# Kernel optimization log

Hardware: AMD Instinct MI355X
Metric: run time of the kernel (lower is better)

The kernel has to match this reference:

```python
import jax, jax.numpy as jnp
import numpy as np
import math

EMBED_DIM = 1024
NUM_HEADS = 16
HEAD_DIM = EMBED_DIM // NUM_HEADS
BLOCK_SIZE = 64
N_GLOBAL = 8


def _sparse_mask(seq_len: int) -> jnp.ndarray:
    """Block-diagonal local mask + 8 global tokens (rows and cols), bool [S, S]."""
    idx = jnp.arange(seq_len)
    block_id = idx // BLOCK_SIZE
    local = block_id[:, None] == block_id[None, :]
    # torch.linspace(0, S-1, min(8, S)).long() -> truncated evenly spaced positions
    gp = np.linspace(0, seq_len - 1, min(N_GLOBAL, seq_len)).astype(np.int64)
    is_global = jnp.zeros((seq_len,), dtype=bool).at[jnp.asarray(gp)].set(True)
    return local | is_global[:, None] | is_global[None, :]


def setup_inputs() -> dict:
    key = jax.random.key(0)
    ks = jax.random.split(key, 9)
    E = EMBED_DIM
    s = 0.02
    return {
        "x": jax.random.normal(ks[0], (1, 4096, E), dtype=jnp.float32),
        "Wq": jax.random.normal(ks[1], (E, E), dtype=jnp.float32) * s,
        "bq": jnp.zeros((E,), dtype=jnp.float32),
        "Wk": jax.random.normal(ks[2], (E, E), dtype=jnp.float32) * s,
        "bk": jnp.zeros((E,), dtype=jnp.float32),
        "Wv": jax.random.normal(ks[3], (E, E), dtype=jnp.float32) * s,
        "bv": jnp.zeros((E,), dtype=jnp.float32),
        "Wo": jax.random.normal(ks[4], (E, E), dtype=jnp.float32) * s,
        "bo": jnp.zeros((E,), dtype=jnp.float32),
    }


def reference(x, Wq, bq, Wk, bk, Wv, bv, Wo, bo):
    B, S, E = x.shape
    H, D = NUM_HEADS, HEAD_DIM
    mask = _sparse_mask(S)  # [S, S] bool

    def split_heads(y):
        return y.reshape(B, S, H, D).transpose(0, 2, 1, 3)  # [B,H,S,D]

    q = split_heads(x @ Wq + bq)
    k = split_heads(x @ Wk + bk)
    v = split_heads(x @ Wv + bv)

    scale = math.sqrt(D)
    scores = jnp.einsum("bhqd,bhkd->bhqk", q, k) / scale  # [B,H,S,S]
    scores = jnp.where(mask[None, None], scores, -jnp.inf)
    attn = jax.nn.softmax(scores, axis=-1)  # every row has its diagonal block -> no NaN
    out = jnp.einsum("bhqk,bhkd->bhqd", attn, v)
    out = out.transpose(0, 2, 1, 3).reshape(B, S, E)
    return out @ Wo + bo
```

## Files before the change

### kernel.cpp

```cpp
#include <hip/hip_runtime.h>

typedef __attribute__((ext_vector_type(8))) short short8;
typedef __attribute__((ext_vector_type(8))) __bf16 bf16x8;
typedef __attribute__((ext_vector_type(4))) float f32x4;

#define S_LEN 4096
#define EMB   1024
#define NHEAD 16
#define HDIM  64
#define GCHUNK 256
#define NCHUNK (S_LEN / GCHUNK)

__constant__ int GPOS[8] = {0, 585, 1170, 1755, 2340, 2925, 3510, 4095};

__device__ __forceinline__ unsigned short f2bf(float f) {
    unsigned int u = __float_as_uint(f);
    u += 0x7fffu + ((u >> 16) & 1u);
    return (unsigned short)(u >> 16);
}
__device__ __forceinline__ float bf2f(unsigned short s) {
    return __uint_as_float(((unsigned int)s) << 16);
}
#define GLOAD16(src, dst) __builtin_amdgcn_global_load_lds( \
    (const __attribute__((address_space(1))) void*)(src),    \
    (__attribute__((address_space(3))) void*)(dst), 16, 0, 0)

__global__ __launch_bounds__(256) void convert_x_kernel(const float4* __restrict__ in,
                                                        ushort4* __restrict__ out, int n4) {
    for (int i = blockIdx.x * blockDim.x + threadIdx.x; i < n4; i += gridDim.x * blockDim.x) {
        float4 v = in[i];
        ushort4 o;
        o.x = f2bf(v.x); o.y = f2bf(v.y); o.z = f2bf(v.z); o.w = f2bf(v.w);
        out[i] = o;
    }
}

__global__ __launch_bounds__(256) void convert_w_kernel(const float* __restrict__ W0,
                                                        const float* __restrict__ W1,
                                                        const float* __restrict__ W2,
                                                        const float* __restrict__ W3,
                                                        unsigned short* __restrict__ wt) {
    __shared__ float tile[64][65];
    const int bx = blockIdx.x;
    const int w = bx >> 8, rem = bx & 255;
    const int k0 = (rem >> 4) * 64, n0 = (rem & 15) * 64;
    const float* W = (w == 0) ? W0 : (w == 1) ? W1 : (w == 2) ? W2 : W3;
    unsigned short* dst = wt + (size_t)w * (1u << 20);
    const int t = threadIdx.x;
    for (int i = t; i < 4096; i += 256) {
        int r = i >> 6, c = i & 63;
        tile[r][c] = W[(size_t)(k0 + r) * EMB + n0 + c];
    }
    __syncthreads();
    for (int i = t; i < 4096; i += 256) {
        int r = i >> 6, c = i & 63;
        dst[(size_t)(n0 + r) * EMB + k0 + c] = f2bf(tile[c][r]);
    }
}

__global__ __launch_bounds__(256) void vtrans(const unsigned short* __restrict__ vb,
                                              unsigned short* __restrict__ vtg) {
    __shared__ unsigned short tile[64][72];
    const int t = threadIdx.x;
    const int h = blockIdx.x >> 6;
    const int s0 = (blockIdx.x & 63) * 64;
    for (int i = t; i < 512; i += 256) {
        int r = i >> 3, c = i & 7;
        *(short8*)&tile[r][c * 8] = *(const short8*)(vb + (size_t)(s0 + r) * EMB + h * 64 + c * 8);
    }
    __syncthreads();
    for (int i = t; i < 512; i += 256) {
        int d = i >> 3, c = i & 7;
        short8 v;
#pragma unroll
        for (int j = 0; j < 8; ++j) v[j] = (short)tile[c * 8 + j][d];
        *(short8*)(vtg + (size_t)(h * 64 + d) * S_LEN + s0 + c * 8) = v;
    }
}

__global__ __launch_bounds__(256) void gemm_qkv(const unsigned short* __restrict__ A,
                                                const unsigned short* __restrict__ Bt,
                                                const float* __restrict__ bq,
                                                const float* __restrict__ bk,
                                                const float* __restrict__ bv,
                                                unsigned short* __restrict__ qb,
                                                unsigned short* __restrict__ kb,
                                                unsigned short* __restrict__ vb) {
    __shared__ unsigned short As[2][128 * 64];
    __shared__ unsigned short Bs[2][128 * 64];
    const int t = threadIdx.x;
    const int lane = t & 63;
    const int wave = t >> 6;
    const int wm = wave >> 1, wn = wave & 1;
    const int col16 = lane & 15, grp = lane >> 4;
    const int bm = blockIdx.x / 24;
    const int bn = blockIdx.x % 24;
    const int sel = bn >> 3, bn_l = bn & 7;
    const float* bias = (sel == 0) ? bq : (sel == 1) ? bk : bv;
    unsigned short* out = (sel == 0) ? qb : (sel == 1) ? kb : vb;

    f32x4 acc[4][4] = {};

    auto stage = [&](int buf, int tstep) {
        const int k0 = tstep * 64;
#pragma unroll
        for (int c = 0; c < 4; ++c) {
            int p = t + 256 * c;
            int row = p >> 3, s = p & 7, kc = s ^ (row & 7);
            GLOAD16(A + (size_t)(bm * 128 + row) * EMB + k0 + kc * 8, &As[buf][p * 8]);
        }
#pragma unroll
        for (int c = 0; c < 4; ++c) {
            int p = t + 256 * c;
            int row = p >> 3, s = p & 7, kc = s ^ (row & 7);
            GLOAD16(Bt + (size_t)(bn * 128 + row) * EMB + k0 + kc * 8, &Bs[buf][p * 8]);
        }
    };

    auto compute = [&](int cur) {
        const unsigned short* Ab = As[cur];
        const unsigned short* Bb = Bs[cur];
#pragma unroll
        for (int kk = 0; kk < 2; ++kk) {
            const int kc = kk * 4 + grp;
            bf16x8 af[4], bfr[4];
#pragma unroll
            for (int f = 0; f < 4; ++f) {
                int mrow = wm * 64 + f * 16 + col16;
                short8 ra = *(const short8*)(Ab + (mrow * 8 + (kc ^ (mrow & 7))) * 8);
                af[f] = __builtin_bit_cast(bf16x8, ra);
                int nrow = wn * 64 + f * 16 + col16;
                short8 rb = *(const short8*)(Bb + (nrow * 8 + (kc ^ (nrow & 7))) * 8);
                bfr[f] = __builtin_bit_cast(bf16x8, rb);
            }
#pragma unroll
            for (int fi = 0; fi < 4; ++fi)
#pragma unroll
                for (int fj = 0; fj < 4; ++fj)
                    acc[fi][fj] = __builtin_amdgcn_mfma_f32_16x16x32_bf16(af[fi], bfr[fj], acc[fi][fj], 0, 0, 0);
        }
    };

    stage(0, 0);
    stage(1, 1);

#pragma unroll 2
    for (int tstep = 0; tstep < 14; ++tstep) {
        const int cur = tstep & 1;
        asm volatile("s_waitcnt vmcnt(8)" ::: "memory");
        __builtin_amdgcn_s_barrier();
        compute(cur);
        __builtin_amdgcn_s_barrier();
        stage(cur, tstep + 2);
    }
    asm volatile("s_waitcnt vmcnt(8)" ::: "memory");
    __builtin_amdgcn_s_barrier();
    compute(0);
    asm volatile("s_waitcnt vmcnt(0)" ::: "memory");
    __builtin_amdgcn_s_barrier();
    compute(1);

#pragma unroll
    for (int fi = 0; fi < 4; ++fi) {
        const int row0 = bm * 128 + wm * 64 + fi * 16 + grp * 4;
#pragma unroll
        for (int fj = 0; fj < 4; ++fj) {
            const int col = bn_l * 128 + wn * 64 + fj * 16 + col16;
            const float bvv = bias[col];
#pragma unroll
            for (int r = 0; r < 4; ++r)
                out[(size_t)(row0 + r) * EMB + col] = f2bf(acc[fi][fj][r] + bvv);
        }
    }
}

__global__ __launch_bounds__(256) void gemm_out(const unsigned short* __restrict__ A,
                                                const unsigned short* __restrict__ Bt,
                                                const float* __restrict__ bias,
                                                float* __restrict__ Cout) {
    __shared__ unsigned short As[2][128 * 64];
    __shared__ unsigned short Bs[2][128 * 64];
    const int t = threadIdx.x;
    const int lane = t & 63;
    const int wave = t >> 6;
    const int wm = wave >> 1, wn = wave & 1;
    const int col16 = lane & 15, grp = lane >> 4;
    const int bm = blockIdx.x >> 3;
    const int bn = blockIdx.x & 7;

    f32x4 acc[4][4] = {};

    auto stage = [&](int buf, int tstep) {
        const int k0 = tstep * 64;
#pragma unroll
        for (int c = 0; c < 4; ++c) {
            int p = t + 256 * c;
            int row = p >> 3, s = p & 7, kc = s ^ (row & 7);
            GLOAD16(A + (size_t)(bm * 128 + row) * EMB + k0 + kc * 8, &As[buf][p * 8]);
        }
#pragma unroll
        for (int c = 0; c < 4; ++c) {
            int p = t + 256 * c;
            int row = p >> 3, s = p & 7, kc = s ^ (row & 7);
            GLOAD16(Bt + (size_t)(bn * 128 + row) * EMB + k0 + kc * 8, &Bs[buf][p * 8]);
        }
    };

    auto compute = [&](int cur) {
        const unsigned short* Ab = As[cur];
        const unsigned short* Bb = Bs[cur];
#pragma unroll
        for (int kk = 0; kk < 2; ++kk) {
            const int kc = kk * 4 + grp;
            bf16x8 af[4], bfr[4];
#pragma unroll
            for (int f = 0; f < 4; ++f) {
                int mrow = wm * 64 + f * 16 + col16;
                short8 ra = *(const short8*)(Ab + (mrow * 8 + (kc ^ (mrow & 7))) * 8);
                af[f] = __builtin_bit_cast(bf16x8, ra);
                int nrow = wn * 64 + f * 16 + col16;
                short8 rb = *(const short8*)(Bb + (nrow * 8 + (kc ^ (nrow & 7))) * 8);
                bfr[f] = __builtin_bit_cast(bf16x8, rb);
            }
#pragma unroll
            for (int fi = 0; fi < 4; ++fi)
#pragma unroll
                for (int fj = 0; fj < 4; ++fj)
                    acc[fi][fj] = __builtin_amdgcn_mfma_f32_16x16x32_bf16(af[fi], bfr[fj], acc[fi][fj], 0, 0, 0);
        }
    };

    stage(0, 0);
    stage(1, 1);

#pragma unroll 2
    for (int tstep = 0; tstep < 14; ++tstep) {
        const int cur = tstep & 1;
        asm volatile("s_waitcnt vmcnt(8)" ::: "memory");
        __builtin_amdgcn_s_barrier();
        compute(cur);
        __builtin_amdgcn_s_barrier();
        stage(cur, tstep + 2);
    }
    asm volatile("s_waitcnt vmcnt(8)" ::: "memory");
    __builtin_amdgcn_s_barrier();
    compute(0);
    asm volatile("s_waitcnt vmcnt(0)" ::: "memory");
    __builtin_amdgcn_s_barrier();
    compute(1);

#pragma unroll
    for (int fi = 0; fi < 4; ++fi) {
        const int row0 = bm * 128 + wm * 64 + fi * 16 + grp * 4;
#pragma unroll
        for (int fj = 0; fj < 4; ++fj) {
            const int col = bn * 128 + wn * 64 + fj * 16 + col16;
            const float bvv = bias[col];
#pragma unroll
            for (int r = 0; r < 4; ++r)
                Cout[(size_t)(row0 + r) * EMB + col] = acc[fi][fj][r] + bvv;
        }
    }
}

__global__ __launch_bounds__(256) void attn_local(const unsigned short* __restrict__ qb,
                                                  const unsigned short* __restrict__ kb,
                                                  const unsigned short* __restrict__ vb,
                                                  const unsigned short* __restrict__ vtg,
                                                  unsigned short* __restrict__ ab) {
    __shared__ unsigned short Qs[64 * 64];
    __shared__ unsigned short Ks[80 * 64];
    __shared__ unsigned short Vts[64 * 64];
    __shared__ unsigned short Ps[64 * 64];
    __shared__ float Pg[64][9];
    __shared__ float Vg[8][64];

    const int t = threadIdx.x;
    const int lane = t & 63, wave = t >> 6;
    const int col16 = lane & 15, grp = lane >> 4;
    const int h = blockIdx.x >> 6, b = blockIdx.x & 63;
    const int bc = h * 64;

#pragma unroll
    for (int c = 0; c < 2; ++c) {
        int p = t + 256 * c, row = p >> 3, s = p & 7, kc = s ^ (row & 7);
        GLOAD16(qb + (size_t)(b * 64 + row) * EMB + bc + kc * 8, Qs + p * 8);
    }
#pragma unroll
    for (int c = 0; c < 3; ++c) {
        int p = t + 256 * c;
        if (p < 576) {
            int row = p >> 3, s = p & 7, kc = s ^ (row & 7);
            int srow = (row < 64) ? (b * 64 + row) : GPOS[row - 64];
            GLOAD16(kb + (size_t)srow * EMB + bc + kc * 8, Ks + p * 8);
        }
    }
    if (t < 64) {
        short8 z = {};
        *(short8*)(Ks + (576 + t) * 8) = z;
    }
#pragma unroll
    for (int c = 0; c < 2; ++c) {
        int p = t + 256 * c, row = p >> 3, s = p & 7, kc = s ^ (row & 7);
        GLOAD16(vtg + (size_t)(bc + row) * S_LEN + b * 64 + kc * 8, Vts + p * 8);
    }
    for (int i = t; i < 512; i += 256) {
        int g = i >> 6, d = i & 63;
        Vg[g][d] = bf2f(vb[(size_t)GPOS[g] * EMB + bc + d]);
    }
    asm volatile("s_waitcnt vmcnt(0)" ::: "memory");
    __syncthreads();

    f32x4 sc[5] = {};
    const int arow = wave * 16 + col16;
#pragma unroll
    for (int kk = 0; kk < 2; ++kk) {
        const int kc = kk * 4 + (lane >> 4);
        short8 ra = *(const short8*)(Qs + (arow * 8 + (kc ^ (arow & 7))) * 8);
        bf16x8 af = __builtin_bit_cast(bf16x8, ra);
#pragma unroll
        for (int n = 0; n < 5; ++n) {
            const int brow = n * 16 + col16;
            short8 rb = *(const short8*)(Ks + (brow * 8 + (kc ^ (brow & 7))) * 8);
            sc[n] = __builtin_amdgcn_mfma_f32_16x16x32_bf16(af, __builtin_bit_cast(bf16x8, rb), sc[n], 0, 0, 0);
        }
    }

    const bool valid4 = (col16 < 8) && ((GPOS[col16] >> 6) != b);
#pragma unroll
    for (int r = 0; r < 4; ++r) {
        const int row = wave * 16 + grp * 4 + r;
        float s[5];
#pragma unroll
        for (int n = 0; n < 4; ++n) s[n] = sc[n][r] * 0.125f;
        s[4] = valid4 ? sc[4][r] * 0.125f : -1e30f;
        float m = fmaxf(fmaxf(fmaxf(s[0], s[1]), fmaxf(s[2], s[3])), s[4]);
#pragma unroll
        for (int off = 1; off < 16; off <<= 1) m = fmaxf(m, __shfl_xor(m, off));
        float e[5], l = 0.f;
#pragma unroll
        for (int n = 0; n < 5; ++n) { e[n] = __expf(s[n] - m); l += e[n]; }
#pragma unroll
        for (int off = 1; off < 16; off <<= 1) l += __shfl_xor(l, off);
        const float inv = 1.f / l;
#pragma unroll
        for (int n = 0; n < 4; ++n) {
            const int col = n * 16 + col16;
            const int kc = col >> 3;
            Ps[(row * 8 + (kc ^ (row & 7))) * 8 + (col & 7)] = f2bf(e[n] * inv);
        }
        if (col16 < 8) Pg[row][col16] = e[4] * inv;
    }
    __syncthreads();

    f32x4 oa[4] = {};
#pragma unroll
    for (int kk = 0; kk < 2; ++kk) {
        const int kc = kk * 4 + (lane >> 4);
        short8 ra = *(const short8*)(Ps + (arow * 8 + (kc ^ (arow & 7))) * 8);
        bf16x8 af = __builtin_bit_cast(bf16x8, ra);
#pragma unroll
        for (int n = 0; n < 4; ++n) {
            const int drow = n * 16 + col16;
            short8 rb = *(const short8*)(Vts + (drow * 8 + (kc ^ (drow & 7))) * 8);
            oa[n] = __builtin_amdgcn_mfma_f32_16x16x32_bf16(af, __builtin_bit_cast(bf16x8, rb), oa[n], 0, 0, 0);
        }
    }

    float pgr[4][8];
#pragma unroll
    for (int r = 0; r < 4; ++r) {
        const int row = wave * 16 + grp * 4 + r;
#pragma unroll
        for (int g = 0; g < 8; ++g) pgr[r][g] = Pg[row][g];
    }
#pragma unroll
    for (int n = 0; n < 4; ++n) {
        const int d = n * 16 + col16;
#pragma unroll
        for (int g = 0; g < 8; ++g) {
            const float vg = Vg[g][d];
#pragma unroll
            for (int r = 0; r < 4; ++r) oa[n][r] += pgr[r][g] * vg;
        }
    }

#pragma unroll
    for (int n = 0; n < 4; ++n) {
        const int d = n * 16 + col16;
#pragma unroll
        for (int r = 0; r < 4; ++r) {
            const int row = wave * 16 + grp * 4 + r;
            ab[(size_t)(b * 64 + row) * EMB + bc + d] = f2bf(oa[n][r]);
        }
    }
}

__global__ __launch_bounds__(256) void attn_gpart(const unsigned short* __restrict__ qb,
                                                  const unsigned short* __restrict__ kb,
                                                  const unsigned short* __restrict__ vb,
                                                  float* __restrict__ o_part,
                                                  float* __restrict__ m_l) {
    __shared__ float Qs[8][64];
    __shared__ unsigned short Vs[GCHUNK][64];
    __shared__ float Ps[8][GCHUNK];
    __shared__ float mfin[8], lfin[8];
    const int t = threadIdx.x;
    const int lane = t & 63;
    const int wave = t >> 6;
    const int h = blockIdx.x >> 4;
    const int ch = blockIdx.x & (NCHUNK - 1);
    const int bc = h * 64;
    const int k0 = ch * GCHUNK;

    for (int i = t; i < 512; i += 256) {
        int r = i >> 6, d = i & 63;
        Qs[r][d] = bf2f(qb[(size_t)GPOS[r] * EMB + bc + d]);
    }
    {
        const unsigned short* vrow = vb + (size_t)(k0 + t) * EMB + bc;
#pragma unroll
        for (int c = 0; c < 8; ++c) {
            short8 vv = *(const short8*)(vrow + c * 8);
            *(short8*)(&Vs[t][(c ^ (t & 7)) * 8]) = vv;
        }
    }
    float kf[64];
    {
        const unsigned short* krow = kb + (size_t)(k0 + t) * EMB + bc;
#pragma unroll
        for (int c = 0; c < 8; ++c) {
            short8 kv = *(const short8*)(krow + c * 8);
#pragma unroll
            for (int j = 0; j < 8; ++j) kf[c * 8 + j] = bf2f((unsigned short)kv[j]);
        }
    }
    __syncthreads();

#pragma unroll
    for (int r = 0; r < 8; ++r) {
        float a0 = 0.f, a1 = 0.f, a2 = 0.f, a3 = 0.f;
#pragma unroll
        for (int c4 = 0; c4 < 16; ++c4) {
            f32x4 q = *(const f32x4*)&Qs[r][c4 * 4];
            a0 += q.x * kf[c4 * 4 + 0];
            a1 += q.y * kf[c4 * 4 + 1];
            a2 += q.z * kf[c4 * 4 + 2];
            a3 += q.w * kf[c4 * 4 + 3];
        }
        Ps[r][t] = (a0 + a1 + a2 + a3) * 0.125f;
    }
    __syncthreads();

#pragma unroll
    for (int rr = 0; rr < 2; ++rr) {
        const int r = wave * 2 + rr;
        float v0 = Ps[r][lane], v1 = Ps[r][lane + 64], v2 = Ps[r][lane + 128], v3 = Ps[r][lane + 192];
        float m = fmaxf(fmaxf(v0, v1), fmaxf(v2, v3));
#pragma unroll
        for (int off = 1; off < 64; off <<= 1) m = fmaxf(m, __shfl_xor(m, off));
        float e0 = __expf(v0 - m), e1 = __expf(v1 - m), e2 = __expf(v2 - m), e3 = __expf(v3 - m);
        float l = e0 + e1 + e2 + e3;
#pragma unroll
        for (int off = 1; off < 64; off <<= 1) l += __shfl_xor(l, off);
        Ps[r][lane] = e0; Ps[r][lane + 64] = e1; Ps[r][lane + 128] = e2; Ps[r][lane + 192] = e3;
        if (lane == 0) { mfin[r] = m; lfin[r] = l; }
    }
    __syncthreads();

    const int r = t >> 5;
    const int d0 = (t & 31) * 2;
    const int cc = d0 >> 3, ee = d0 & 7;
    float acc0 = 0.f, acc1 = 0.f;
    for (int k = 0; k < GCHUNK; k += 4) {
        f32x4 p = *(const f32x4*)&Ps[r][k];
#pragma unroll
        for (int j = 0; j < 4; ++j) {
            unsigned int vv = *(const unsigned int*)&Vs[k + j][((cc ^ ((k + j) & 7)) << 3) + ee];
            acc0 += p[j] * bf2f((unsigned short)(vv & 0xffff));
            acc1 += p[j] * bf2f((unsigned short)(vv >> 16));
        }
    }
    const int rowg = h * 8 + r;
    float* od = o_part + ((size_t)rowg * NCHUNK + ch) * 64 + d0;
    od[0] = acc0; od[1] = acc1;
    if ((t & 31) == 0) {
        m_l[((size_t)rowg * NCHUNK + ch) * 2 + 0] = mfin[r];
        m_l[((size_t)rowg * NCHUNK + ch) * 2 + 1] = lfin[r];
    }
}

__global__ __launch_bounds__(256) void attn_gcomb(const float* __restrict__ o_part,
                                                  const float* __restrict__ m_l,
                                                  unsigned short* __restrict__ ab) {
    const int gid = blockIdx.x * 256 + threadIdx.x;
    const int row = gid >> 6, d = gid & 63;
    float M = -1e30f;
#pragma unroll
    for (int c = 0; c < NCHUNK; ++c) M = fmaxf(M, m_l[((size_t)row * NCHUNK + c) * 2]);
    float L = 0.f, o = 0.f;
#pragma unroll
    for (int c = 0; c < NCHUNK; ++c) {
        float w = __expf(m_l[((size_t)row * NCHUNK + c) * 2] - M);
        L += m_l[((size_t)row * NCHUNK + c) * 2 + 1] * w;
        o += o_part[((size_t)row * NCHUNK + c) * 64 + d] * w;
    }
    const int h = row >> 3, gi = row & 7;
    ab[(size_t)GPOS[gi] * EMB + h * 64 + d] = f2bf(o / L);
}

extern "C" void kernel_launch(void* const* d_in, const int* in_sizes, int n_in,
                              void* d_out, int out_size, void* d_ws, size_t ws_size,
                              hipStream_t stream) {
    const float* x  = (const float*)d_in[0];
    const float* Wq = (const float*)d_in[1];
    const float* bq = (const float*)d_in[2];
    const float* Wk = (const float*)d_in[3];
    const float* bk = (const float*)d_in[4];
    const float* Wv = (const float*)d_in[5];
    const float* bv = (const float*)d_in[6];
    const float* Wo = (const float*)d_in[7];
    const float* bo = (const float*)d_in[8];

    char* ws = (char*)d_ws;
    unsigned short* xb = (unsigned short*)ws;
    unsigned short* wt = (unsigned short*)(ws + (8u << 20));
    unsigned short* qb = (unsigned short*)(ws + (16u << 20));
    unsigned short* kb = (unsigned short*)(ws + (24u << 20));
    unsigned short* vb = (unsigned short*)(ws + (32u << 20));
    unsigned short* ab = xb;

    float* o_part = (float*)d_out;
    float* m_l    = (float*)d_out + 128 * NCHUNK * 64;
    unsigned short* vtg = (unsigned short*)((char*)d_out + (4u << 20));

    const int n4 = S_LEN * EMB / 4;
    convert_x_kernel<<<2048, 256, 0, stream>>>((const float4*)x, (ushort4*)xb, n4);
    convert_w_kernel<<<1024, 256, 0, stream>>>(Wq, Wk, Wv, Wo, wt);

    gemm_qkv<<<(S_LEN / 128) * 24, 256, 0, stream>>>(xb, wt, bq, bk, bv, qb, kb, vb);

    vtrans<<<1024, 256, 0, stream>>>(vb, vtg);
    attn_local<<<NHEAD * 64, 256, 0, stream>>>(qb, kb, vb, vtg, ab);
    attn_gpart<<<NHEAD * NCHUNK, 256, 0, stream>>>(qb, kb, vb, o_part, m_l);
    attn_gcomb<<<(128 * 64) / 256, 256, 0, stream>>>(o_part, m_l, ab);

    gemm_out<<<(S_LEN / 128) * 8, 256, 0, stream>>>(ab, wt + (3u << 20), bo, (float*)d_out);
}
```

Measured before the change: 101.2 us.

## Fuse conversions, V transpose into QKV epilogue, and attention kernels

Merges the x and weight conversion kernels into one launch, folds the V transpose into the QKV GEMM epilogue via a swizzled LDS tile, and merges local and global-row attention kernels into one grid branching on block index. This removes three kernel launches, the separate vtrans pass over V, and lets the small global-attention work overlap with local attention. The fused attention kernel uses a shared LDS buffer sized for the larger path, which may affect occupancy, and V blocks of the GEMM do extra LDS work and stores.

```diff
diff --git a/kernel.cpp b/kernel.cpp
--- a/kernel.cpp
+++ b/kernel.cpp
@@ -25,56 +25,39 @@
     (const __attribute__((address_space(1))) void*)(src),    \
     (__attribute__((address_space(3))) void*)(dst), 16, 0, 0)
 
-__global__ __launch_bounds__(256) void convert_x_kernel(const float4* __restrict__ in,
-                                                        ushort4* __restrict__ out, int n4) {
-    for (int i = blockIdx.x * blockDim.x + threadIdx.x; i < n4; i += gridDim.x * blockDim.x) {
-        float4 v = in[i];
-        ushort4 o;
-        o.x = f2bf(v.x); o.y = f2bf(v.y); o.z = f2bf(v.z); o.w = f2bf(v.w);
-        out[i] = o;
-    }
-}
-
-__global__ __launch_bounds__(256) void convert_w_kernel(const float* __restrict__ W0,
-                                                        const float* __restrict__ W1,
-                                                        const float* __restrict__ W2,
-                                                        const float* __restrict__ W3,
-                                                        unsigned short* __restrict__ wt) {
+__global__ __launch_bounds__(256) void convert_all(const float* __restrict__ x,
+                                                   const float* __restrict__ W0,
+                                                   const float* __restrict__ W1,
+                                                   const float* __restrict__ W2,
+                                                   const float* __restrict__ W3,
+                                                   ushort4* __restrict__ xb,
+                                                   unsigned short* __restrict__ wt) {
     __shared__ float tile[64][65];
-    const int bx = blockIdx.x;
-    const int w = bx >> 8, rem = bx & 255;
-    const int k0 = (rem >> 4) * 64, n0 = (rem & 15) * 64;
-    const float* W = (w == 0) ? W0 : (w == 1) ? W1 : (w == 2) ? W2 : W3;
-    unsigned short* dst = wt + (size_t)w * (1u << 20);
     const int t = threadIdx.x;
-    for (int i = t; i < 4096; i += 256) {
-        int r = i >> 6, c = i & 63;
-        tile[r][c] = W[(size_t)(k0 + r) * EMB + n0 + c];
-    }
-    __syncthreads();
-    for (int i = t; i < 4096; i += 256) {
-        int r = i >> 6, c = i & 63;
-        dst[(size_t)(n0 + r) * EMB + k0 + c] = f2bf(tile[c][r]);
-    }
-}
-
-__global__ __launch_bounds__(256) void vtrans(const unsigned short* __restrict__ vb,
-                                              unsigned short* __restrict__ vtg) {
-    __shared__ unsigned short tile[64][72];
-    const int t = threadIdx.x;
-    const int h = blockIdx.x >> 6;
-    const int s0 = (blockIdx.x & 63) * 64;
-    for (int i = t; i < 512; i += 256) {
-        int r = i >> 3, c = i & 7;
-        *(short8*)&tile[r][c * 8] = *(const short8*)(vb + (size_t)(s0 + r) * EMB + h * 64 + c * 8);
-    }
-    __syncthreads();
-    for (int i = t; i < 512; i += 256) {
-        int d = i >> 3, c = i & 7;
-        short8 v;
-#pragma unroll
-        for (int j = 0; j < 8; ++j) v[j] = (short)tile[c * 8 + j][d];
-        *(short8*)(vtg + (size_t)(h * 64 + d) * S_LEN + s0 + c * 8) = v;
+    if (blockIdx.x < 1024) {
+        const int bx = blockIdx.x;
+        const int w = bx >> 8, rem = bx & 255;
+        const int k0 = (rem >> 4) * 64, n0 = (rem & 15) * 64;
+        const float* W = (w == 0) ? W0 : (w == 1) ? W1 : (w == 2) ? W2 : W3;
+        unsigned short* dst = wt + (size_t)w * (1u << 20);
+        for (int i = t; i < 4096; i += 256) {
+            int r = i >> 6, c = i & 63;
+            tile[r][c] = W[(size_t)(k0 + r) * EMB + n0 + c];
+        }
+        __syncthreads();
+        for (int i = t; i < 4096; i += 256) {
+            int r = i >> 6, c = i & 63;
+            dst[(size_t)(n0 + r) * EMB + k0 + c] = f2bf(tile[c][r]);
+        }
+    } else {
+        const int n4 = S_LEN * EMB / 4;
+        const float4* in = (const float4*)x;
+        for (int i = (blockIdx.x - 1024) * 256 + t; i < n4; i += 2048 * 256) {
+            float4 v = in[i];
+            ushort4 o;
+            o.x = f2bf(v.x); o.y = f2bf(v.y); o.z = f2bf(v.z); o.w = f2bf(v.w);
+            xb[i] = o;
+        }
     }
 }
 
@@ -85,7 +68,8 @@
                                                 const float* __restrict__ bv,
                                                 unsigned short* __restrict__ qb,
                                                 unsigned short* __restrict__ kb,
-                                                unsigned short* __restrict__ vb) {
+                                                unsigned short* __restrict__ vb,
+                                                unsigned short* __restrict__ vtg) {
     __shared__ unsigned short As[2][128 * 64];
     __shared__ unsigned short Bs[2][128 * 64];
     const int t = threadIdx.x;
@@ -170,6 +154,31 @@
 #pragma unroll
             for (int r = 0; r < 4; ++r)
                 out[(size_t)(row0 + r) * EMB + col] = f2bf(acc[fi][fj][r] + bvv);
+        }
+    }
+
+    if (sel == 2) {
+        __syncthreads();
+        unsigned short* T = &As[0][0];
+#pragma unroll
+        for (int fi = 0; fi < 4; ++fi) {
+            const int row_l = wm * 64 + fi * 16 + grp * 4;
+#pragma unroll
+            for (int fj = 0; fj < 4; ++fj) {
+                const int col_l = wn * 64 + fj * 16 + col16;
+                const float bvv = bias[bn_l * 128 + col_l];
+#pragma unroll
+                for (int r = 0; r < 4; ++r)
+                    T[col_l * 128 + ((row_l + r) ^ ((col_l & 15) << 3))] = f2bf(acc[fi][fj][r] + bvv);
+            }
+        }
+        __syncthreads();
+#pragma unroll
+        for (int c = 0; c < 8; ++c) {
+            int q = t + 256 * c;
+            int col = q >> 4, sc = q & 15, s0 = sc * 8;
+            short8 v = *(const short8*)(T + col * 128 + (s0 ^ ((col & 15) << 3)));
+            *(short8*)(vtg + (size_t)(bn_l * 128 + col) * S_LEN + bm * 128 + s0) = v;
         }
     }
 }
@@ -263,230 +272,232 @@
     }
 }
 
-__global__ __launch_bounds__(256) void attn_local(const unsigned short* __restrict__ qb,
+__global__ __launch_bounds__(256) void attn_fused(const unsigned short* __restrict__ qb,
                                                   const unsigned short* __restrict__ kb,
                                                   const unsigned short* __restrict__ vb,
                                                   const unsigned short* __restrict__ vtg,
-                                                  unsigned short* __restrict__ ab) {
-    __shared__ unsigned short Qs[64 * 64];
-    __shared__ unsigned short Ks[80 * 64];
-    __shared__ unsigned short Vts[64 * 64];
-    __shared__ unsigned short Ps[64 * 64];
-    __shared__ float Pg[64][9];
-    __shared__ float Vg[8][64];
-
+                                                  unsigned short* __restrict__ ab,
+                                                  float* __restrict__ o_part,
+                                                  float* __restrict__ m_l) {
+    __shared__ __align__(16) char smem[43072];
     const int t = threadIdx.x;
     const int lane = t & 63, wave = t >> 6;
-    const int col16 = lane & 15, grp = lane >> 4;
-    const int h = blockIdx.x >> 6, b = blockIdx.x & 63;
-    const int bc = h * 64;
-
-#pragma unroll
-    for (int c = 0; c < 2; ++c) {
-        int p = t + 256 * c, row = p >> 3, s = p & 7, kc = s ^ (row & 7);
-        GLOAD16(qb + (size_t)(b * 64 + row) * EMB + bc + kc * 8, Qs + p * 8);
-    }
-#pragma unroll
-    for (int c = 0; c < 3; ++c) {
-        int p = t + 256 * c;
-        if (p < 576) {
-            int row = p >> 3, s = p & 7, kc = s ^ (row & 7);
-            int srow = (row < 64) ? (b * 64 + row) : GPOS[row - 64];
-            GLOAD16(kb + (size_t)srow * EMB + bc + kc * 8, Ks + p * 8);
-        }
-    }
-    if (t < 64) {
-        short8 z = {};
-        *(short8*)(Ks + (576 + t) * 8) = z;
-    }
-#pragma unroll
-    for (int c = 0; c < 2; ++c) {
-        int p = t + 256 * c, row = p >> 3, s = p & 7, kc = s ^ (row & 7);
-        GLOAD16(vtg + (size_t)(bc + row) * S_LEN + b * 64 + kc * 8, Vts + p * 8);
-    }
-    for (int i = t; i < 512; i += 256) {
-        int g = i >> 6, d = i & 63;
-        Vg[g][d] = bf2f(vb[(size_t)GPOS[g] * EMB + bc + d]);
-    }
-    asm volatile("s_waitcnt vmcnt(0)" ::: "memory");
-    __syncthreads();
-
-    f32x4 sc[5] = {};
-    const int arow = wave * 16 + col16;
-#pragma unroll
-    for (int kk = 0; kk < 2; ++kk) {
-        const int kc = kk * 4 + (lane >> 4);
-        short8 ra = *(const short8*)(Qs + (arow * 8 + (kc ^ (arow & 7))) * 8);
-        bf16x8 af = __builtin_bit_cast(bf16x8, ra);
-#pragma unroll
-        for (int n = 0; n < 5; ++n) {
-            const int brow = n * 16 + col16;
-            short8 rb = *(const short8*)(Ks + (brow * 8 + (kc ^ (brow & 7))) * 8);
-            sc[n] = __builtin_amdgcn_mfma_f32_16x16x32_bf16(af, __builtin_bit_cast(bf16x8, rb), sc[n], 0, 0, 0);
-        }
-    }
-
-    const bool valid4 = (col16 < 8) && ((GPOS[col16] >> 6) != b);
-#pragma unroll
-    for (int r = 0; r < 4; ++r) {
-        const int row = wave * 16 + grp * 4 + r;
-        float s[5];
-#pragma unroll
-        for (int n = 0; n < 4; ++n) s[n] = sc[n][r] * 0.125f;
-        s[4] = valid4 ? sc[4][r] * 0.125f : -1e30f;
-        float m = fmaxf(fmaxf(fmaxf(s[0], s[1]), fmaxf(s[2], s[3])), s[4]);
-#pragma unroll
-        for (int off = 1; off < 16; off <<= 1) m = fmaxf(m, __shfl_xor(m, off));
-        float e[5], l = 0.f;
-#pragma unroll
-        for (int n = 0; n < 5; ++n) { e[n] = __expf(s[n] - m); l += e[n]; }
-#pragma unroll
-        for (int off = 1; off < 16; off <<= 1) l += __shfl_xor(l, off);
-        const float inv = 1.f / l;
-#pragma unroll
-        for (int n = 0; n < 4; ++n) {
-            const int col = n * 16 + col16;
-            const int kc = col >> 3;
-            Ps[(row * 8 + (kc ^ (row & 7))) * 8 + (col & 7)] = f2bf(e[n] * inv);
-        }
-        if (col16 < 8) Pg[row][col16] = e[4] * inv;
-    }
-    __syncthreads();
-
-    f32x4 oa[4] = {};
-#pragma unroll
-    for (int kk = 0; kk < 2; ++kk) {
-        const int kc = kk * 4 + (lane >> 4);
-        short8 ra = *(const short8*)(Ps + (arow * 8 + (kc ^ (arow & 7))) * 8);
-        bf16x8 af = __builtin_bit_cast(bf16x8, ra);
-#pragma unroll
-        for (int n = 0; n < 4; ++n) {
-            const int drow = n * 16 + col16;
-            short8 rb = *(const short8*)(Vts + (drow * 8 + (kc ^ (drow & 7))) * 8);
-            oa[n] = __builtin_amdgcn_mfma_f32_16x16x32_bf16(af, __builtin_bit_cast(bf16x8, rb), oa[n], 0, 0, 0);
-        }
-    }
-
-    float pgr[4][8];
-#pragma unroll
-    for (int r = 0; r < 4; ++r) {
-        const int row = wave * 16 + grp * 4 + r;
-#pragma unroll
-        for (int g = 0; g < 8; ++g) pgr[r][g] = Pg[row][g];
-    }
-#pragma unroll
-    for (int n = 0; n < 4; ++n) {
-        const int d = n * 16 + col16;
-#pragma unroll
-        for (int g = 0; g < 8; ++g) {
-            const float vg = Vg[g][d];
-#pragma unroll
-            for (int r = 0; r < 4; ++r) oa[n][r] += pgr[r][g] * vg;
-        }
-    }
-
-#pragma unroll
-    for (int n = 0; n < 4; ++n) {
-        const int d = n * 16 + col16;
+
+    if (blockIdx.x < 1024) {
+        unsigned short* Qs  = (unsigned short*)smem;
+        unsigned short* Ks  = Qs + 64 * 64;
+        unsigned short* Vts = Ks + 80 * 64;
+        unsigned short* Ps  = Vts + 64 * 64;
+        float* Pg = (float*)(Ps + 64 * 64);
+        float* Vg = Pg + 64 * 9;
+
+        const int col16 = lane & 15, grp = lane >> 4;
+        const int h = blockIdx.x >> 6, b = blockIdx.x & 63;
+        const int bc = h * 64;
+
+#pragma unroll
+        for (int c = 0; c < 2; ++c) {
+            int p = t + 256 * c, row = p >> 3, s = p & 7, kc = s ^ (row & 7);
+            GLOAD16(qb + (size_t)(b * 64 + row) * EMB + bc + kc * 8, Qs + p * 8);
+        }
+#pragma unroll
+        for (int c = 0; c < 3; ++c) {
+            int p = t + 256 * c;
+            if (p < 576) {
+                int row = p >> 3, s = p & 7, kc = s ^ (row & 7);
+                int srow = (row < 64) ? (b * 64 + row) : GPOS[row - 64];
+                GLOAD16(kb + (size_t)srow * EMB + bc + kc * 8, Ks + p * 8);
+            }
+        }
+        if (t < 64) {
+            short8 z = {};
+            *(short8*)(Ks + (576 + t) * 8) = z;
+        }
+#pragma unroll
+        for (int c = 0; c < 2; ++c) {
+            int p = t + 256 * c, row = p >> 3, s = p & 7, kc = s ^ (row & 7);
+            GLOAD16(vtg + (size_t)(bc + row) * S_LEN + b * 64 + kc * 8, Vts + p * 8);
+        }
+        for (int i = t; i < 512; i += 256) {
+            int g = i >> 6, d = i & 63;
+            Vg[g * 64 + d] = bf2f(vb[(size_t)GPOS[g] * EMB + bc + d]);
+        }
+        asm volatile("s_waitcnt vmcnt(0)" ::: "memory");
+        __syncthreads();
+
+        f32x4 sc[5] = {};
+        const int arow = wave * 16 + col16;
+#pragma unroll
+        for (int kk = 0; kk < 2; ++kk) {
+            const int kc = kk * 4 + grp;
+            short8 ra = *(const short8*)(Qs + (arow * 8 + (kc ^ (arow & 7))) * 8);
+            bf16x8 af = __builtin_bit_cast(bf16x8, ra);
+#pragma unroll
+            for (int n = 0; n < 5; ++n) {
+                const int brow = n * 16 + col16;
+                short8 rb = *(const short8*)(Ks + (brow * 8 + (kc ^ (brow & 7))) * 8);
+                sc[n] = __builtin_amdgcn_mfma_f32_16x16x32_bf16(af, __builtin_bit_cast(bf16x8, rb), sc[n], 0, 0, 0);
+            }
+        }
+
+        const bool valid4 = (col16 < 8) && ((GPOS[col16] >> 6) != b);
 #pragma unroll
         for (int r = 0; r < 4; ++r) {
             const int row = wave * 16 + grp * 4 + r;
-            ab[(size_t)(b * 64 + row) * EMB + bc + d] = f2bf(oa[n][r]);
-        }
-    }
-}
-
-__global__ __launch_bounds__(256) void attn_gpart(const unsigned short* __restrict__ qb,
-                                                  const unsigned short* __restrict__ kb,
-                                                  const unsigned short* __restrict__ vb,
-                                                  float* __restrict__ o_part,
-                                                  float* __restrict__ m_l) {
-    __shared__ float Qs[8][64];
-    __shared__ unsigned short Vs[GCHUNK][64];
-    __shared__ float Ps[8][GCHUNK];
-    __shared__ float mfin[8], lfin[8];
-    const int t = threadIdx.x;
-    const int lane = t & 63;
-    const int wave = t >> 6;
-    const int h = blockIdx.x >> 4;
-    const int ch = blockIdx.x & (NCHUNK - 1);
-    const int bc = h * 64;
-    const int k0 = ch * GCHUNK;
-
-    for (int i = t; i < 512; i += 256) {
-        int r = i >> 6, d = i & 63;
-        Qs[r][d] = bf2f(qb[(size_t)GPOS[r] * EMB + bc + d]);
-    }
-    {
-        const unsigned short* vrow = vb + (size_t)(k0 + t) * EMB + bc;
-#pragma unroll
-        for (int c = 0; c < 8; ++c) {
-            short8 vv = *(const short8*)(vrow + c * 8);
-            *(short8*)(&Vs[t][(c ^ (t & 7)) * 8]) = vv;
-        }
-    }
-    float kf[64];
-    {
-        const unsigned short* krow = kb + (size_t)(k0 + t) * EMB + bc;
-#pragma unroll
-        for (int c = 0; c < 8; ++c) {
-            short8 kv = *(const short8*)(krow + c * 8);
-#pragma unroll
-            for (int j = 0; j < 8; ++j) kf[c * 8 + j] = bf2f((unsigned short)kv[j]);
-        }
-    }
-    __syncthreads();
-
-#pragma unroll
-    for (int r = 0; r < 8; ++r) {
-        float a0 = 0.f, a1 = 0.f, a2 = 0.f, a3 = 0.f;
-#pragma unroll
-        for (int c4 = 0; c4 < 16; ++c4) {
-            f32x4 q = *(const f32x4*)&Qs[r][c4 * 4];
-            a0 += q.x * kf[c4 * 4 + 0];
-            a1 += q.y * kf[c4 * 4 + 1];
-            a2 += q.z * kf[c4 * 4 + 2];
-            a3 += q.w * kf[c4 * 4 + 3];
-        }
-        Ps[r][t] = (a0 + a1 + a2 + a3) * 0.125f;
-    }
-    __syncthreads();
-
-#pragma unroll
-    for (int rr = 0; rr < 2; ++rr) {
-        const int r = wave * 2 + rr;
-        float v0 = Ps[r][lane], v1 = Ps[r][lane + 64], v2 = Ps[r][lane + 128], v3 = Ps[r][lane + 192];
-        float m = fmaxf(fmaxf(v0, v1), fmaxf(v2, v3));
-#pragma unroll
-        for (int off = 1; off < 64; off <<= 1) m = fmaxf(m, __shfl_xor(m, off));
-        float e0 = __expf(v0 - m), e1 = __expf(v1 - m), e2 = __expf(v2 - m), e3 = __expf(v3 - m);
-        float l = e0 + e1 + e2 + e3;
-#pragma unroll
-        for (int off = 1; off < 64; off <<= 1) l += __shfl_xor(l, off);
-        Ps[r][lane] = e0; Ps[r][lane + 64] = e1; Ps[r][lane + 128] = e2; Ps[r][lane + 192] = e3;
-        if (lane == 0) { mfin[r] = m; lfin[r] = l; }
-    }
-    __syncthreads();
-
-    const int r = t >> 5;
-    const int d0 = (t & 31) * 2;
-    const int cc = d0 >> 3, ee = d0 & 7;
-    float acc0 = 0.f, acc1 = 0.f;
-    for (int k = 0; k < GCHUNK; k += 4) {
-        f32x4 p = *(const f32x4*)&Ps[r][k];
-#pragma unroll
-        for (int j = 0; j < 4; ++j) {
-            unsigned int vv = *(const unsigned int*)&Vs[k + j][((cc ^ ((k + j) & 7)) << 3) + ee];
-            acc0 += p[j] * bf2f((unsigned short)(vv & 0xffff));
-            acc1 += p[j] * bf2f((unsigned short)(vv >> 16));
-        }
-    }
-    const int rowg = h * 8 + r;
-    float* od = o_part + ((size_t)rowg * NCHUNK + ch) * 64 + d0;
-    od[0] = acc0; od[1] = acc1;
-    if ((t & 31) == 0) {
-        m_l[((size_t)rowg * NCHUNK + ch) * 2 + 0] = mfin[r];
-        m_l[((size_t)rowg * NCHUNK + ch) * 2 + 1] = lfin[r];
+            float s[5];
+#pragma unroll
+            for (int n = 0; n < 4; ++n) s[n] = sc[n][r] * 0.125f;
+            s[4] = valid4 ? sc[4][r] * 0.125f : -1e30f;
+            float m = fmaxf(fmaxf(fmaxf(s[0], s[1]), fmaxf(s[2], s[3])), s[4]);
+#pragma unroll
+            for (int off = 1; off < 16; off <<= 1) m = fmaxf(m, __shfl_xor(m, off));
+            float e[5], l = 0.f;
+#pragma unroll
+            for (int n = 0; n < 5; ++n) { e[n] = __expf(s[n] - m); l += e[n]; }
+#pragma unroll
+            for (int off = 1; off < 16; off <<= 1) l += __shfl_xor(l, off);
+            const float inv = 1.f / l;
+#pragma unroll
+            for (int n = 0; n < 4; ++n) {
+                const int col = n * 16 + col16;
+                const int kc = col >> 3;
+                Ps[(row * 8 + (kc ^ (row & 7))) * 8 + (col & 7)] = f2bf(e[n] * inv);
+            }
+            if (col16 < 8) Pg[row * 9 + col16] = e[4] * inv;
+        }
+        __syncthreads();
+
+        f32x4 oa[4] = {};
+#pragma unroll
+        for (int kk = 0; kk < 2; ++kk) {
+            const int kc = kk * 4 + grp;
+            short8 ra = *(const short8*)(Ps + (arow * 8 + (kc ^ (arow & 7))) * 8);
+            bf16x8 af = __builtin_bit_cast(bf16x8, ra);
+#pragma unroll
+            for (int n = 0; n < 4; ++n) {
+                const int drow = n * 16 + col16;
+                short8 rb = *(const short8*)(Vts + (drow * 8 + (kc ^ (drow & 7))) * 8);
+                oa[n] = __builtin_amdgcn_mfma_f32_16x16x32_bf16(af, __builtin_bit_cast(bf16x8, rb), oa[n], 0, 0, 0);
+            }
+        }
+
+        float pgr[4][8];
+#pragma unroll
+        for (int r = 0; r < 4; ++r) {
+            const int row = wave * 16 + grp * 4 + r;
+#pragma unroll
+            for (int g = 0; g < 8; ++g) pgr[r][g] = Pg[row * 9 + g];
+        }
+#pragma unroll
+        for (int n = 0; n < 4; ++n) {
+            const int d = n * 16 + col16;
+#pragma unroll
+            for (int g = 0; g < 8; ++g) {
+                const float vg = Vg[g * 64 + d];
+#pragma unroll
+                for (int r = 0; r < 4; ++r) oa[n][r] += pgr[r][g] * vg;
+            }
+        }
+
+#pragma unroll
+        for (int n = 0; n < 4; ++n) {
+            const int d = n * 16 + col16;
+#pragma unroll
+            for (int r = 0; r < 4; ++r) {
+                const int row = wave * 16 + grp * 4 + r;
+                ab[(size_t)(b * 64 + row) * EMB + bc + d] = f2bf(oa[n][r]);
+            }
+        }
+    } else {
+        float* Qsf = (float*)smem;
+        unsigned short* Vs = (unsigned short*)(smem + 2048);
+        float* Ps = (float*)(smem + 2048 + 32768);
+        float* mfin = Ps + 8 * 256;
+        float* lfin = mfin + 8;
+
+        const int bx = blockIdx.x - 1024;
+        const int h = bx >> 4;
+        const int ch = bx & (NCHUNK - 1);
+        const int bc = h * 64;
+        const int k0 = ch * GCHUNK;
+
+        for (int i = t; i < 512; i += 256) {
+            int r = i >> 6, d = i & 63;
+            Qsf[r * 64 + d] = bf2f(qb[(size_t)GPOS[r] * EMB + bc + d]);
+        }
+        {
+            const unsigned short* vrow = vb + (size_t)(k0 + t) * EMB + bc;
+#pragma unroll
+            for (int c = 0; c < 8; ++c) {
+                short8 vv = *(const short8*)(vrow + c * 8);
+                *(short8*)(&Vs[t * 64 + (c ^ (t & 7)) * 8]) = vv;
+            }
+        }
+        float kf[64];
+        {
+            const unsigned short* krow = kb + (size_t)(k0 + t) * EMB + bc;
+#pragma unroll
+            for (int c = 0; c < 8; ++c) {
+                short8 kv = *(const short8*)(krow + c * 8);
+#pragma unroll
+                for (int j = 0; j < 8; ++j) kf[c * 8 + j] = bf2f((unsigned short)kv[j]);
+            }
+        }
+        __syncthreads();
+
+#pragma unroll
+        for (int r = 0; r < 8; ++r) {
+            float a0 = 0.f, a1 = 0.f, a2 = 0.f, a3 = 0.f;
+#pragma unroll
+            for (int c4 = 0; c4 < 16; ++c4) {
+                f32x4 q = *(const f32x4*)&Qsf[r * 64 + c4 * 4];
+                a0 += q.x * kf[c4 * 4 + 0];
+                a1 += q.y * kf[c4 * 4 + 1];
+                a2 += q.z * kf[c4 * 4 + 2];
+                a3 += q.w * kf[c4 * 4 + 3];
+            }
+            Ps[r * 256 + t] = (a0 + a1 + a2 + a3) * 0.125f;
+        }
+        __syncthreads();
+
+#pragma unroll
+        for (int rr = 0; rr < 2; ++rr) {
+            const int r = wave * 2 + rr;
+            float v0 = Ps[r * 256 + lane], v1 = Ps[r * 256 + lane + 64],
+                  v2 = Ps[r * 256 + lane + 128], v3 = Ps[r * 256 + lane + 192];
+            float m = fmaxf(fmaxf(v0, v1), fmaxf(v2, v3));
+#pragma unroll
+            for (int off = 1; off < 64; off <<= 1) m = fmaxf(m, __shfl_xor(m, off));
+            float e0 = __expf(v0 - m), e1 = __expf(v1 - m), e2 = __expf(v2 - m), e3 = __expf(v3 - m);
+            float l = e0 + e1 + e2 + e3;
+#pragma unroll
+            for (int off = 1; off < 64; off <<= 1) l += __shfl_xor(l, off);
+            Ps[r * 256 + lane] = e0; Ps[r * 256 + lane + 64] = e1;
+            Ps[r * 256 + lane + 128] = e2; Ps[r * 256 + lane + 192] = e3;
+            if (lane == 0) { mfin[r] = m; lfin[r] = l; }
+        }
+        __syncthreads();
+
+        const int r = t >> 5;
+        const int d0 = (t & 31) * 2;
+        const int cc = d0 >> 3, ee = d0 & 7;
+        float acc0 = 0.f, acc1 = 0.f;
+        for (int k = 0; k < GCHUNK; k += 4) {
+            f32x4 p = *(const f32x4*)&Ps[r * 256 + k];
+#pragma unroll
+            for (int j = 0; j < 4; ++j) {
+                unsigned int vv = *(const unsigned int*)&Vs[(k + j) * 64 + ((cc ^ ((k + j) & 7)) << 3) + ee];
+                acc0 += p[j] * bf2f((unsigned short)(vv & 0xffff));
+                acc1 += p[j] * bf2f((unsigned short)(vv >> 16));
+            }
+        }
+        const int rowg = h * 8 + r;
+        float* od = o_part + ((size_t)rowg * NCHUNK + ch) * 64 + d0;
+        od[0] = acc0; od[1] = acc1;
+        if ((t & 31) == 0) {
+            m_l[((size_t)rowg * NCHUNK + ch) * 2 + 0] = mfin[r];
+            m_l[((size_t)rowg * NCHUNK + ch) * 2 + 1] = lfin[r];
+        }
     }
 }
 
@@ -534,15 +545,11 @@
     float* m_l    = (float*)d_out + 128 * NCHUNK * 64;
     unsigned short* vtg = (unsigned short*)((char*)d_out + (4u << 20));
 
-    const int n4 = S_LEN * EMB / 4;
-    convert_x_kernel<<<2048, 256, 0, stream>>>((const float4*)x, (ushort4*)xb, n4);
-    convert_w_kernel<<<1024, 256, 0, stream>>>(Wq, Wk, Wv, Wo, wt);
-
-    gemm_qkv<<<(S_LEN / 128) * 24, 256, 0, stream>>>(xb, wt, bq, bk, bv, qb, kb, vb);
-
-    vtrans<<<1024, 256, 0, stream>>>(vb, vtg);
-    attn_local<<<NHEAD * 64, 256, 0, stream>>>(qb, kb, vb, vtg, ab);
-    attn_gpart<<<NHEAD * NCHUNK, 256, 0, stream>>>(qb, kb, vb, o_part, m_l);
+    convert_all<<<3072, 256, 0, stream>>>(x, Wq, Wk, Wv, Wo, (ushort4*)xb, wt);
+
+    gemm_qkv<<<(S_LEN / 128) * 24, 256, 0, stream>>>(xb, wt, bq, bk, bv, qb, kb, vb, vtg);
+
+    attn_fused<<<1024 + NHEAD * NCHUNK, 256, 0, stream>>>(qb, kb, vb, vtg, ab, o_part, m_l);
     attn_gcomb<<<(128 * 64) / 256, 256, 0, stream>>>(o_part, m_l, ab);
 
     gemm_out<<<(S_LEN / 128) * 8, 256, 0, stream>>>(ab, wt + (3u << 20), bo, (float*)d_out);
```

Result: faster. 91.67 us (-9.4%).
